# Performance work log

Measured on AMD Instinct MI355X. Metric: run time of the kernel, lower is better.

The kernel has to match this reference:

```python
import jax, jax.numpy as jnp
import numpy as np

N_NODES = 100000
N_EDGES = 1600000
HIDDEN = 128
NUM_CLASSES = 10
NUM_LAYERS = 4
NUM_GRAPHS = 200
BN_EPS = 1e-5


def setup_inputs() -> dict:
    key = jax.random.key(0)
    ks = jax.random.split(key, 16)
    s = 1.0 / np.sqrt(HIDDEN)
    inp = {
        "x": jax.random.normal(ks[0], (N_NODES, HIDDEN), jnp.float32),
        "edge_index": jax.random.randint(ks[1], (2, N_EDGES), 0, N_NODES, jnp.int64),
        "batch": jnp.sort(jax.random.randint(ks[2], (N_NODES,), 0, NUM_GRAPHS, jnp.int64)),
        # GatedGraphConv per-layer message weights [L, H, H]
        "ggnn_weight": jax.random.uniform(ks[3], (NUM_LAYERS, HIDDEN, HIDDEN), jnp.float32, -s, s),
        # shared GRUCell params (torch layout: [3H, H])
        "gru_w_ih": jax.random.uniform(ks[4], (3 * HIDDEN, HIDDEN), jnp.float32, -s, s),
        "gru_w_hh": jax.random.uniform(ks[5], (3 * HIDDEN, HIDDEN), jnp.float32, -s, s),
        "gru_b_ih": jax.random.uniform(ks[6], (3 * HIDDEN,), jnp.float32, -s, s),
        "gru_b_hh": jax.random.uniform(ks[7], (3 * HIDDEN,), jnp.float32, -s, s),
        "fc1_w": jax.random.uniform(ks[8], (HIDDEN, HIDDEN), jnp.float32, -s, s),
        "fc1_b": jax.random.uniform(ks[9], (HIDDEN,), jnp.float32, -s, s),
        "bn_gamma": jnp.ones((HIDDEN,), jnp.float32),
        "bn_beta": jnp.zeros((HIDDEN,), jnp.float32),
        "fc2_w": jax.random.uniform(ks[10], (NUM_CLASSES, HIDDEN), jnp.float32, -s, s),
        "fc2_b": jax.random.uniform(ks[11], (NUM_CLASSES,), jnp.float32, -s, s),
    }
    return inp


def _gru_cell(m, h, w_ih, w_hh, b_ih, b_hh):
    gi = m @ w_ih.T + b_ih  # [N, 3H]
    gh = h @ w_hh.T + b_hh
    i_r, i_z, i_n = jnp.split(gi, 3, axis=-1)
    h_r, h_z, h_n = jnp.split(gh, 3, axis=-1)
    r = jax.nn.sigmoid(i_r + h_r)
    z = jax.nn.sigmoid(i_z + h_z)
    n = jnp.tanh(i_n + r * h_n)
    return (1.0 - z) * n + z * h


def reference(x, edge_index, batch, ggnn_weight, gru_w_ih, gru_w_hh, gru_b_ih,
              gru_b_hh, fc1_w, fc1_b, bn_gamma, bn_beta, fc2_w, fc2_b):
    src, dst = edge_index[0], edge_index[1]
    h = x
    for l in range(NUM_LAYERS):
        m = h @ ggnn_weight[l]                       # [N, H] per-layer transform
        agg = jax.ops.segment_sum(m[src], dst, num_segments=N_NODES)  # scatter-add
        h = _gru_cell(agg, h, gru_w_ih, gru_w_hh, gru_b_ih, gru_b_hh)
    # fc1 -> batchnorm (training-mode batch stats) -> relu; dropout is identity (eval)
    y = h @ fc1_w.T + fc1_b
    mu = jnp.mean(y, axis=0)
    var = jnp.var(y, axis=0)
    y = (y - mu) * jax.lax.rsqrt(var + BN_EPS) * bn_gamma + bn_beta
    y = jax.nn.relu(y)
    # global mean pool per graph
    sums = jax.ops.segment_sum(y, batch, num_segments=NUM_GRAPHS)
    counts = jax.ops.segment_sum(jnp.ones((N_NODES,), y.dtype), batch, num_segments=NUM_GRAPHS)
    gfeat = sums / jnp.clip(counts, 1.0)[:, None]    # [G, H]
    out = gfeat @ fc2_w.T + fc2_b                    # [G, C]
    return jax.nn.log_softmax(out, axis=-1)
```

## Files before the change

### kernel.cpp

```cpp
#include <hip/hip_runtime.h>
#include <math.h>

#define HID 128
#define NLAYERS 4
#define NGRAPHS 200
#define NCLASSES 10
#define BN_EPS 1e-5f

typedef short bf16x8 __attribute__((ext_vector_type(8)));
typedef float f32x4 __attribute__((ext_vector_type(4)));

__device__ __forceinline__ ushort f2bf(float f) {
    unsigned u = __float_as_uint(f);
    u = (u + 0x7fffu + ((u >> 16) & 1u)) >> 16;
    return (ushort)u;
}
__device__ __forceinline__ float bf2f(unsigned us) { return __uint_as_float(us << 16); }


__global__ void k_init_x(const float* __restrict__ x, ushort* __restrict__ A, int N) {
    int idx = blockIdx.x * blockDim.x + threadIdx.x;
    if (idx < N * HID) {
        int n = idx >> 7, c = idx & 127;
        A[n * 256 + 128 + c] = f2bf(x[idx]);
    }
}

__global__ __launch_bounds__(128) void k_wgemm(const float* __restrict__ W,
                                               const float* __restrict__ w_ih,
                                               float* __restrict__ C) {
    int l = blockIdx.x >> 7, k = blockIdx.x & 127;
    __shared__ float wrow[128];
    wrow[threadIdx.x] = W[(l << 14) + k * 128 + threadIdx.x];
    __syncthreads();
    for (int j = threadIdx.x; j < 384; j += 128) {
        float acc = 0.f;
#pragma unroll 4
        for (int o = 0; o < 128; ++o) acc += wrow[o] * w_ih[j * 128 + o];
        C[((size_t)l * 128 + k) * 384 + j] = acc;
    }
}

__global__ void k_build_Bc(const float* __restrict__ C, const float* __restrict__ w_hh,
                           ushort* __restrict__ Bc2) {
    int idx = blockIdx.x * blockDim.x + threadIdx.x;
    if (idx >= NLAYERS * 512 * 256) return;
    int jf = idx & 7, lane = (idx >> 3) & 63, ks = (idx >> 9) & 7, ct = (idx >> 12) & 31;
    int l = idx >> 17;
    int o = ct * 16 + (lane & 15);
    int k = ks * 32 + (lane >> 4) * 8 + jf;
    float v;
    if (k < 128)      v = (o < 384) ? C[((size_t)l * 128 + k) * 384 + o] : 0.f;
    else if (o < 256) v = w_hh[o * 128 + (k - 128)];
    else if (o < 384) v = 0.f;
    else              v = w_hh[(o - 128) * 128 + (k - 128)];
    Bc2[idx] = f2bf(v);
}

__global__ void k_bias(const float* __restrict__ b_ih, const float* __restrict__ b_hh,
                       float* __restrict__ bias) {
    int j = threadIdx.x;
    if (j >= 512) return;
    float v;
    if (j < 256)      v = b_ih[j] + b_hh[j];
    else if (j < 384) v = b_ih[j];
    else              v = b_hh[j - 128];
    bias[j] = v;
}

__global__ void k_cvt_fc1(const float* __restrict__ w, ushort* __restrict__ B2) {
    int idx = blockIdx.x * blockDim.x + threadIdx.x;
    if (idx >= 16384) return;
    int j = idx & 7, lane = (idx >> 3) & 63, ks = (idx >> 9) & 3, ct = idx >> 11;
    int o = ct * 16 + (lane & 15);
    int k = ks * 32 + (lane >> 4) * 8 + j;
    B2[idx] = f2bf(w[o * 128 + k]);
}


__global__ void k_deg(const int* __restrict__ ei, int E, int* __restrict__ deg) {
    int e = blockIdx.x * blockDim.x + threadIdx.x;
    if (e < E) atomicAdd(&deg[ei[E + e]], 1);
}

__global__ void k_scan1(const int* __restrict__ deg, int N,
                        int* __restrict__ rowstart, int* __restrict__ bsum) {
    __shared__ int s[256];
    int t = threadIdx.x;
    int i = blockIdx.x * 256 + t;
    int v = (i < N) ? deg[i] : 0;
    s[t] = v;
    __syncthreads();
    for (int off = 1; off < 256; off <<= 1) {
        int a = (t >= off) ? s[t - off] : 0;
        __syncthreads();
        s[t] += a;
        __syncthreads();
    }
    if (i < N) rowstart[i] = s[t] - v;
    if (t == 255) bsum[blockIdx.x] = s[255];
}

__global__ void k_scan2(const int* __restrict__ bsum, int nb, int* __restrict__ boff) {
    __shared__ int s[512];
    int t = threadIdx.x;
    int v = (t < nb) ? bsum[t] : 0;
    s[t] = v;
    __syncthreads();
    for (int off = 1; off < 512; off <<= 1) {
        int a = (t >= off) ? s[t - off] : 0;
        __syncthreads();
        s[t] += a;
        __syncthreads();
    }
    if (t < nb) boff[t] = s[t] - v;
}

__global__ void k_scan3(int* __restrict__ rowstart, const int* __restrict__ boff,
                        int N, int E) {
    int i = blockIdx.x * 256 + threadIdx.x;
    if (i < N) rowstart[i] += boff[blockIdx.x];
    if (i == 0) rowstart[N] = E;
}

__global__ void k_fill(const int* __restrict__ ei, int E,
                       const int* __restrict__ rowstart, int* __restrict__ cursor,
                       int* __restrict__ col) {
    int e = blockIdx.x * blockDim.x + threadIdx.x;
    if (e < E) {
        int d = ei[E + e];
        int pos = atomicAdd(&cursor[d], 1);
        col[rowstart[d] + pos] = ei[e];
    }
}


__global__ void k_gstart(const int* __restrict__ batch, int* __restrict__ gstart, int N) {
    int n = blockIdx.x * blockDim.x + threadIdx.x;
    if (n > N) return;
    int curb = (n == N) ? NGRAPHS : batch[n];
    int prev = (n == 0) ? -1 : batch[n - 1];
    for (int g = prev + 1; g <= curb; ++g) gstart[g] = n;
}


__global__ __launch_bounds__(256) void k_gather_bf(const int* __restrict__ rowstart,
                                                   const int* __restrict__ col,
                                                   ushort* __restrict__ A, int N) {
    int node = blockIdx.x * 4 + (threadIdx.x >> 6);
    int lane = threadIdx.x & 63;
    if (node >= N) return;
    int s = rowstart[node], e = rowstart[node + 1];
    int sub = lane >> 4;
    int chunk = lane & 15;
    const ushort* hb = A + 128;
    float acc[8];
#pragma unroll
    for (int k = 0; k < 8; ++k) acc[k] = 0.f;
    int i = s + sub;
    for (; i + 12 < e; i += 16) {
        int c0 = col[i], c1 = col[i + 4], c2 = col[i + 8], c3 = col[i + 12];
        bf16x8 v0 = *(const bf16x8*)(hb + (size_t)c0 * 256 + chunk * 8);
        bf16x8 v1 = *(const bf16x8*)(hb + (size_t)c1 * 256 + chunk * 8);
        bf16x8 v2 = *(const bf16x8*)(hb + (size_t)c2 * 256 + chunk * 8);
        bf16x8 v3 = *(const bf16x8*)(hb + (size_t)c3 * 256 + chunk * 8);
#pragma unroll
        for (int k = 0; k < 8; ++k) {
            acc[k] += bf2f((ushort)v0[k]) + bf2f((ushort)v1[k]);
            acc[k] += bf2f((ushort)v2[k]) + bf2f((ushort)v3[k]);
        }
    }
    for (; i < e; i += 4) {
        int c0 = col[i];
        bf16x8 v0 = *(const bf16x8*)(hb + (size_t)c0 * 256 + chunk * 8);
#pragma unroll
        for (int k = 0; k < 8; ++k) acc[k] += bf2f((ushort)v0[k]);
    }
#pragma unroll
    for (int k = 0; k < 8; ++k) {
        acc[k] += __shfl_xor(acc[k], 16);
        acc[k] += __shfl_xor(acc[k], 32);
    }
    if (sub == 0) {
        union { ushort u[8]; bf16x8 v; } o;
#pragma unroll
        for (int k = 0; k < 8; ++k) o.u[k] = f2bf(acc[k]);
        *(bf16x8*)(A + (size_t)node * 256 + chunk * 8) = o.v;
    }
}


#define LDA 264
__global__ __launch_bounds__(256, 2) void k_gru_mfma(
    const ushort* __restrict__ A, const ushort* __restrict__ Bc2,
    const float* __restrict__ bias, ushort* __restrict__ Ah) {
    __shared__ ushort As[64 * LDA];
    int t = threadIdx.x;
    int rowb = blockIdx.x << 6;
    for (int c = t; c < 2048; c += 256) {
        int r = c >> 5, off = (c & 31) * 8;
        *(bf16x8*)(As + r * LDA + off) =
            *(const bf16x8*)(A + (size_t)(rowb + r) * 256 + off);
    }
    __syncthreads();
    int w = t >> 6, lane = t & 63;
    int quad = lane >> 4, tn = lane & 15;
    f32x4 acc[4][4][2];
#pragma unroll
    for (int rt = 0; rt < 4; ++rt)
#pragma unroll
        for (int g = 0; g < 4; ++g)
#pragma unroll
            for (int c2 = 0; c2 < 2; ++c2) acc[rt][g][c2] = (f32x4){0.f, 0.f, 0.f, 0.f};
    for (int ks = 0; ks < 8; ++ks) {
        int k0 = ks * 32 + quad * 8;
        bf16x8 bfr[4][2];
#pragma unroll
        for (int g = 0; g < 4; ++g)
#pragma unroll
            for (int c2 = 0; c2 < 2; ++c2) {
                int ct = g * 8 + w * 2 + c2;
                bfr[g][c2] = *(const bf16x8*)(Bc2 + (size_t)((ct * 8 + ks) * 64 + lane) * 8);
            }
        bf16x8 af[4];
#pragma unroll
        for (int rt = 0; rt < 4; ++rt)
            af[rt] = *(const bf16x8*)(As + (rt * 16 + tn) * LDA + k0);
#pragma unroll
        for (int rt = 0; rt < 4; ++rt)
#pragma unroll
            for (int g = 0; g < 4; ++g)
#pragma unroll
                for (int c2 = 0; c2 < 2; ++c2)
                    acc[rt][g][c2] = __builtin_amdgcn_mfma_f32_16x16x32_bf16(
                        af[rt], bfr[g][c2], acc[rt][g][c2], 0, 0, 0);
    }
#pragma unroll
    for (int c2 = 0; c2 < 2; ++c2) {
        int cc = w * 32 + c2 * 16 + tn;
        float br = bias[cc], bz = bias[128 + cc], bin = bias[256 + cc], bhn = bias[384 + cc];
#pragma unroll
        for (int rt = 0; rt < 4; ++rt)
#pragma unroll
            for (int r = 0; r < 4; ++r) {
                int rl = rt * 16 + quad * 4 + r;
                int row = rowb + rl;
                float ur = acc[rt][0][c2][r] + br;
                float uz = acc[rt][1][c2][r] + bz;
                float xin = acc[rt][2][c2][r] + bin;
                float xhn = acc[rt][3][c2][r] + bhn;
                float rr = 1.f / (1.f + __expf(-ur));
                float zz = 1.f / (1.f + __expf(-uz));
                float xt = xin + rr * xhn;
                float ex = __expf(2.f * fminf(fmaxf(xt, -15.f), 15.f));
                float nn = (ex - 1.f) / (ex + 1.f);
                float ho = bf2f(As[rl * LDA + 128 + cc]);
                float hv = (1.f - zz) * nn + zz * ho;
                Ah[(size_t)row * 256 + cc] = f2bf(hv);
            }
    }
}


#define LDA2 136
__global__ __launch_bounds__(256, 2) void k_mm_mfma(
    const ushort* __restrict__ Ain, int astride, const ushort* __restrict__ B2,
    ushort* __restrict__ mo) {
    __shared__ ushort As[64 * LDA2];
    int t = threadIdx.x;
    int rowb = blockIdx.x << 6;
    for (int c = t; c < 1024; c += 256) {
        int r = c >> 4, off = (c & 15) * 8;
        *(bf16x8*)(As + r * LDA2 + off) =
            *(const bf16x8*)(Ain + (size_t)(rowb + r) * astride + off);
    }
    __syncthreads();
    int w = t >> 6, lane = t & 63;
    int quad = lane >> 4, tn = lane & 15;
    f32x4 acc[4][2];
#pragma unroll
    for (int rt = 0; rt < 4; ++rt)
#pragma unroll
        for (int c2 = 0; c2 < 2; ++c2) acc[rt][c2] = (f32x4){0.f, 0.f, 0.f, 0.f};
    for (int ks = 0; ks < 4; ++ks) {
        int k0 = ks * 32 + quad * 8;
        bf16x8 bfr[2];
#pragma unroll
        for (int c2 = 0; c2 < 2; ++c2) {
            int ct = w * 2 + c2;
            bfr[c2] = *(const bf16x8*)(B2 + (size_t)((ct * 4 + ks) * 64 + lane) * 8);
        }
        bf16x8 af[4];
#pragma unroll
        for (int rt = 0; rt < 4; ++rt)
            af[rt] = *(const bf16x8*)(As + (rt * 16 + tn) * LDA2 + k0);
#pragma unroll
        for (int rt = 0; rt < 4; ++rt)
#pragma unroll
            for (int c2 = 0; c2 < 2; ++c2)
                acc[rt][c2] = __builtin_amdgcn_mfma_f32_16x16x32_bf16(
                    af[rt], bfr[c2], acc[rt][c2], 0, 0, 0);
    }
#pragma unroll
    for (int c2 = 0; c2 < 2; ++c2) {
        int col = w * 32 + c2 * 16 + tn;
#pragma unroll
        for (int rt = 0; rt < 4; ++rt)
#pragma unroll
            for (int r = 0; r < 4; ++r) {
                int row = rowb + rt * 16 + quad * 4 + r;
                mo[row * 128 + col] = f2bf(acc[rt][c2][r]);
            }
    }
}


__global__ __launch_bounds__(256) void k_bnstats(const ushort* __restrict__ y,
                                                 float* __restrict__ stats, int N) {
    int half = threadIdx.x >> 7, f = threadIdx.x & 127;
    float s = 0.f, s2 = 0.f;
    for (int n = blockIdx.x * 2 + half; n < N; n += gridDim.x * 2) {
        float v = bf2f(y[n * HID + f]);
        s += v;
        s2 += v * v;
    }
    __shared__ float ls[2][HID], ls2[2][HID];
    ls[half][f] = s;
    ls2[half][f] = s2;
    __syncthreads();
    if (half == 0) {
        atomicAdd(&stats[f], ls[0][f] + ls[1][f]);
        atomicAdd(&stats[HID + f], ls2[0][f] + ls2[1][f]);
    }
}

__global__ void k_bnfinal(float* __restrict__ stats, const float* __restrict__ gamma,
                          const float* __restrict__ beta, float n) {
    int j = threadIdx.x;
    if (j < HID) {
        float mu = stats[j] / n;
        float var = stats[HID + j] / n - mu * mu;
        float sc = gamma[j] * rsqrtf(var + BN_EPS);
        stats[256 + j] = sc;
        stats[384 + j] = beta[j] - mu * sc;
    }
}

__global__ __launch_bounds__(256) void k_pool(const ushort* __restrict__ y,
                                              const float* __restrict__ stats,
                                              const int* __restrict__ gstart,
                                              float* __restrict__ gsum) {
    int g = blockIdx.x >> 2, q = blockIdx.x & 3;
    int f = threadIdx.x & 127, half = threadIdx.x >> 7;
    int gs = gstart[g], ge = gstart[g + 1];
    int len = ge - gs;
    int r0 = gs + ((len * q) >> 2), r1 = gs + ((len * (q + 1)) >> 2);
    float sc = stats[256 + f], sh = stats[384 + f];
    float acc = 0.f;
    for (int n = r0 + half; n < r1; n += 2)
        acc += fmaxf(bf2f(y[n * HID + f]) * sc + sh, 0.f);
    __shared__ float ls[2][HID];
    ls[half][f] = acc;
    __syncthreads();
    if (half == 0) atomicAdd(&gsum[g * HID + f], ls[0][f] + ls[1][f]);
}

__global__ void k_head(const float* __restrict__ gsum, const int* __restrict__ gstart,
                       const float* __restrict__ w2, const float* __restrict__ b2,
                       float* __restrict__ out) {
    int g = blockIdx.x * blockDim.x + threadIdx.x;
    if (g >= NGRAPHS) return;
    float cnt = (float)(gstart[g + 1] - gstart[g]);
    float inv = 1.0f / fmaxf(cnt, 1.0f);
    float logits[NCLASSES];
    float mx = -1e30f;
    for (int c = 0; c < NCLASSES; ++c) {
        float acc = b2[c];
        for (int f = 0; f < HID; ++f) acc += gsum[g * HID + f] * inv * w2[c * HID + f];
        logits[c] = acc;
        mx = fmaxf(mx, acc);
    }
    float se = 0.f;
    for (int c = 0; c < NCLASSES; ++c) se += expf(logits[c] - mx);
    float lse = mx + logf(se);
    for (int c = 0; c < NCLASSES; ++c) out[g * NCLASSES + c] = logits[c] - lse;
}


extern "C" void kernel_launch(void* const* d_in, const int* in_sizes, int n_in,
                              void* d_out, int out_size, void* d_ws, size_t ws_size,
                              hipStream_t stream) {
    const float* x     = (const float*)d_in[0];
    const int*   ei    = (const int*)d_in[1];
    const int*   batch = (const int*)d_in[2];
    const float* ggnnw = (const float*)d_in[3];
    const float* w_ih  = (const float*)d_in[4];
    const float* w_hh  = (const float*)d_in[5];
    const float* b_ih  = (const float*)d_in[6];
    const float* b_hh  = (const float*)d_in[7];
    const float* fc1_w = (const float*)d_in[8];
    const float* gamma = (const float*)d_in[10];
    const float* beta  = (const float*)d_in[11];
    const float* fc2_w = (const float*)d_in[12];
    const float* fc2_b = (const float*)d_in[13];
    float* out = (float*)d_out;

    const int N = in_sizes[0] / HID;
    const int E = in_sizes[1] / 2;
    const int nblk64 = (N + 63) / 64;
    const int P = nblk64 * 64;

    char* w = (char*)d_ws;
    auto alloc = [&](size_t bytes) -> char* {
        char* p = w;
        w += (bytes + 255) & ~(size_t)255;
        return p;
    };
    ushort* A   = (ushort*)alloc(sizeof(ushort) * (size_t)P * 256);
    ushort* y   = (ushort*)alloc(sizeof(ushort) * (size_t)P * HID);
    ushort* Bc2 = (ushort*)alloc(sizeof(ushort) * NLAYERS * 512 * 256);
    float*  C   = (float*)alloc(sizeof(float) * NLAYERS * 128 * 384);
    ushort* f1b = (ushort*)alloc(sizeof(ushort) * HID * HID);
    float*  bias = (float*)alloc(sizeof(float) * 512);
    int* rowstart = (int*)alloc(sizeof(int) * (N + 4));
    int* colb     = (int*)alloc(sizeof(int) * E);
    int* bsum     = (int*)alloc(sizeof(int) * 512);
    int* boff     = (int*)alloc(sizeof(int) * 512);
    int* gstart   = (int*)alloc(sizeof(int) * (NGRAPHS + 4));
    size_t zelems = (size_t)N + N + 512 + NGRAPHS * HID;
    char* zbase = alloc(zelems * 4);
    int*   deg    = (int*)zbase;
    int*   cursor = deg + N;
    float* stats  = (float*)(cursor + N);
    float* gsum   = stats + 512;

    hipMemsetAsync(zbase, 0, zelems * 4, stream);

    k_init_x<<<(N * HID + 255) / 256, 256, 0, stream>>>(x, A, N);
    k_wgemm<<<NLAYERS * 128, 128, 0, stream>>>(ggnnw, w_ih, C);
    k_build_Bc<<<(NLAYERS * 512 * 256 + 255) / 256, 256, 0, stream>>>(C, w_hh, Bc2);
    k_bias<<<1, 512, 0, stream>>>(b_ih, b_hh, bias);
    k_cvt_fc1<<<(16384 + 255) / 256, 256, 0, stream>>>(fc1_w, f1b);

    int nb1 = (N + 255) / 256;
    k_deg<<<(E + 255) / 256, 256, 0, stream>>>(ei, E, deg);
    k_scan1<<<nb1, 256, 0, stream>>>(deg, N, rowstart, bsum);
    k_scan2<<<1, 512, 0, stream>>>(bsum, nb1, boff);
    k_scan3<<<nb1, 256, 0, stream>>>(rowstart, boff, N, E);
    k_fill<<<(E + 255) / 256, 256, 0, stream>>>(ei, E, rowstart, cursor, colb);
    k_gstart<<<(N + 256) / 256, 256, 0, stream>>>(batch, gstart, N);

    for (int l = 0; l < NLAYERS; ++l) {
        k_gather_bf<<<(N + 3) / 4, 256, 0, stream>>>(rowstart, colb, A, N);
        k_gru_mfma<<<nblk64, 256, 0, stream>>>(A, Bc2 + (size_t)l * 512 * 256,
                                               bias, A + 128);
    }

    k_mm_mfma<<<nblk64, 256, 0, stream>>>(A + 128, 256, f1b, y);
    k_bnstats<<<512, 256, 0, stream>>>(y, stats, N);
    k_bnfinal<<<1, 128, 0, stream>>>(stats, gamma, beta, (float)N);
    k_pool<<<NGRAPHS * 4, 256, 0, stream>>>(y, stats, gstart, gsum);
    k_head<<<1, 256, 0, stream>>>(gsum, gstart, fc2_w, fc2_b, out);
}
```

Before: 851.0 us.

## Build CSR via two-level bucketed counting sort instead of global atomics

```diff
diff --git a/kernel.cpp b/kernel.cpp
--- a/kernel.cpp
+++ b/kernel.cpp
@@ -78,17 +78,26 @@
 }
 
 
-__global__ void k_deg(const int* __restrict__ ei, int E, int* __restrict__ deg) {
-    int e = blockIdx.x * blockDim.x + threadIdx.x;
-    if (e < E) atomicAdd(&deg[ei[E + e]], 1);
-}
-
-__global__ void k_scan1(const int* __restrict__ deg, int N,
-                        int* __restrict__ rowstart, int* __restrict__ bsum) {
+#define CHUNK 4096
+
+__global__ __launch_bounds__(256) void k_bhist(const int* __restrict__ ei, int E,
+                                               int nb, int* __restrict__ bhist) {
+    __shared__ int lh[256];
+    int t = threadIdx.x;
+    lh[t] = 0;
+    __syncthreads();
+    int base = blockIdx.x * CHUNK;
+    int end = min(base + CHUNK, E);
+    for (int i = base + t; i < end; i += 256) atomicAdd(&lh[ei[E + i] >> 9], 1);
+    __syncthreads();
+    if (t < nb && lh[t]) atomicAdd(&bhist[t], lh[t]);
+}
+
+__global__ void k_bscan(const int* __restrict__ bhist, int nb, int* __restrict__ bstart,
+                        int* __restrict__ bcur, int E) {
     __shared__ int s[256];
     int t = threadIdx.x;
-    int i = blockIdx.x * 256 + t;
-    int v = (i < N) ? deg[i] : 0;
+    int v = (t < nb) ? bhist[t] : 0;
     s[t] = v;
     __syncthreads();
     for (int off = 1; off < 256; off <<= 1) {
@@ -97,41 +106,90 @@
         s[t] += a;
         __syncthreads();
     }
-    if (i < N) rowstart[i] = s[t] - v;
-    if (t == 255) bsum[blockIdx.x] = s[255];
-}
-
-__global__ void k_scan2(const int* __restrict__ bsum, int nb, int* __restrict__ boff) {
-    __shared__ int s[512];
+    if (t < nb) { int ex = s[t] - v; bstart[t] = ex; bcur[t] = ex; }
+    if (t == 0) bstart[nb] = E;
+}
+
+__global__ __launch_bounds__(256) void k_binfill(const int* __restrict__ ei, int E,
+                                                 int nb, int* __restrict__ bcur,
+                                                 int2* __restrict__ binned) {
+    __shared__ int eh[256], eoff[256], ecur[256], gbase[256];
+    __shared__ int2 sbuf[CHUNK];
     int t = threadIdx.x;
-    int v = (t < nb) ? bsum[t] : 0;
-    s[t] = v;
+    eh[t] = 0; ecur[t] = 0;
+    __syncthreads();
+    int base = blockIdx.x * CHUNK;
+    int cnt = min(CHUNK, E - base);
+    int2 ed[16];
+    int nmine = 0;
+    for (int i = t; i < cnt; i += 256) {
+        int s = ei[base + i], d = ei[E + base + i];
+        ed[nmine++] = make_int2(s, d);
+        atomicAdd(&eh[d >> 9], 1);
+    }
+    __syncthreads();
+    int v = eh[t];
+    eoff[t] = v;
+    __syncthreads();
+    for (int off = 1; off < 256; off <<= 1) {
+        int a = (t >= off) ? eoff[t - off] : 0;
+        __syncthreads();
+        eoff[t] += a;
+        __syncthreads();
+    }
+    int excl = eoff[t] - v;
+    __syncthreads();
+    eoff[t] = excl;
+    __syncthreads();
+    for (int j = 0; j < nmine; ++j) {
+        int b = ed[j].y >> 9;
+        int slot = eoff[b] + atomicAdd(&ecur[b], 1);
+        sbuf[slot] = ed[j];
+    }
+    __syncthreads();
+    if (t < nb && eh[t]) gbase[t] = atomicAdd(&bcur[t], eh[t]);
+    __syncthreads();
+    for (int i = t; i < cnt; i += 256) {
+        int2 e = sbuf[i];
+        int b = e.y >> 9;
+        binned[gbase[b] + (i - eoff[b])] = e;
+    }
+}
+
+__global__ __launch_bounds__(256) void k_csr512(const int2* __restrict__ binned,
+                                                const int* __restrict__ bstart,
+                                                int* __restrict__ rowstart,
+                                                int* __restrict__ col, int N, int E) {
+    __shared__ int h[512], cur[512], sc[512];
+    int t = threadIdx.x, b = blockIdx.x;
+    int es = bstart[b], ee = bstart[b + 1];
+    for (int i = t; i < 512; i += 256) h[i] = 0;
+    __syncthreads();
+    for (int i = es + t; i < ee; i += 256) atomicAdd(&h[binned[i].y & 511], 1);
+    __syncthreads();
+    for (int i = t; i < 512; i += 256) sc[i] = h[i];
     __syncthreads();
     for (int off = 1; off < 512; off <<= 1) {
-        int a = (t >= off) ? s[t - off] : 0;
+        int i0 = t, i1 = t + 256;
+        int a0 = (i0 >= off) ? sc[i0 - off] : 0;
+        int a1 = (i1 >= off) ? sc[i1 - off] : 0;
         __syncthreads();
-        s[t] += a;
+        sc[i0] += a0; sc[i1] += a1;
         __syncthreads();
     }
-    if (t < nb) boff[t] = s[t] - v;
-}
-
-__global__ void k_scan3(int* __restrict__ rowstart, const int* __restrict__ boff,
-                        int N, int E) {
-    int i = blockIdx.x * 256 + threadIdx.x;
-    if (i < N) rowstart[i] += boff[blockIdx.x];
-    if (i == 0) rowstart[N] = E;
-}
-
-__global__ void k_fill(const int* __restrict__ ei, int E,
-                       const int* __restrict__ rowstart, int* __restrict__ cursor,
-                       int* __restrict__ col) {
-    int e = blockIdx.x * blockDim.x + threadIdx.x;
-    if (e < E) {
-        int d = ei[E + e];
-        int pos = atomicAdd(&cursor[d], 1);
-        col[rowstart[d] + pos] = ei[e];
-    }
+    for (int i = t; i < 512; i += 256) {
+        int excl = sc[i] - h[i];
+        cur[i] = excl;
+        int node = (b << 9) + i;
+        if (node < N) rowstart[node] = es + excl;
+    }
+    __syncthreads();
+    for (int i = es + t; i < ee; i += 256) {
+        int2 e = binned[i];
+        int p = atomicAdd(&cur[e.y & 511], 1);
+        col[es + p] = e.x;
+    }
+    if (b == 0 && t == 0) rowstart[N] = E;
 }
 
 
@@ -409,6 +467,7 @@
     const int E = in_sizes[1] / 2;
     const int nblk64 = (N + 63) / 64;
     const int P = nblk64 * 64;
+    const int nbuck = (N + 511) >> 9;
 
     char* w = (char*)d_ws;
     auto alloc = [&](size_t bytes) -> char* {
@@ -418,20 +477,20 @@
     };
     ushort* A   = (ushort*)alloc(sizeof(ushort) * (size_t)P * 256);
     ushort* y   = (ushort*)alloc(sizeof(ushort) * (size_t)P * HID);
+    int2*   binned = (int2*)y;
     ushort* Bc2 = (ushort*)alloc(sizeof(ushort) * NLAYERS * 512 * 256);
     float*  C   = (float*)alloc(sizeof(float) * NLAYERS * 128 * 384);
     ushort* f1b = (ushort*)alloc(sizeof(ushort) * HID * HID);
     float*  bias = (float*)alloc(sizeof(float) * 512);
     int* rowstart = (int*)alloc(sizeof(int) * (N + 4));
     int* colb     = (int*)alloc(sizeof(int) * E);
-    int* bsum     = (int*)alloc(sizeof(int) * 512);
-    int* boff     = (int*)alloc(sizeof(int) * 512);
+    int* bstart   = (int*)alloc(sizeof(int) * (nbuck + 4));
+    int* bcur     = (int*)alloc(sizeof(int) * (nbuck + 4));
     int* gstart   = (int*)alloc(sizeof(int) * (NGRAPHS + 4));
-    size_t zelems = (size_t)N + N + 512 + NGRAPHS * HID;
+    size_t zelems = (size_t)nbuck + 512 + NGRAPHS * HID;
     char* zbase = alloc(zelems * 4);
-    int*   deg    = (int*)zbase;
-    int*   cursor = deg + N;
-    float* stats  = (float*)(cursor + N);
+    int*   bhist  = (int*)zbase;
+    float* stats  = (float*)(bhist + nbuck);
     float* gsum   = stats + 512;
 
     hipMemsetAsync(zbase, 0, zelems * 4, stream);
@@ -442,12 +501,11 @@
     k_bias<<<1, 512, 0, stream>>>(b_ih, b_hh, bias);
     k_cvt_fc1<<<(16384 + 255) / 256, 256, 0, stream>>>(fc1_w, f1b);
 
-    int nb1 = (N + 255) / 256;
-    k_deg<<<(E + 255) / 256, 256, 0, stream>>>(ei, E, deg);
-    k_scan1<<<nb1, 256, 0, stream>>>(deg, N, rowstart, bsum);
-    k_scan2<<<1, 512, 0, stream>>>(bsum, nb1, boff);
-    k_scan3<<<nb1, 256, 0, stream>>>(rowstart, boff, N, E);
-    k_fill<<<(E + 255) / 256, 256, 0, stream>>>(ei, E, rowstart, cursor, colb);
+    int nchunk = (E + CHUNK - 1) / CHUNK;
+    k_bhist<<<nchunk, 256, 0, stream>>>(ei, E, nbuck, bhist);
+    k_bscan<<<1, 256, 0, stream>>>(bhist, nbuck, bstart, bcur, E);
+    k_binfill<<<nchunk, 256, 0, stream>>>(ei, E, nbuck, bcur, binned);
+    k_csr512<<<nbuck, 256, 0, stream>>>(binned, bstart, rowstart, colb, N, E);
     k_gstart<<<(N + 256) / 256, 256, 0, stream>>>(batch, gstart, N);
 
     for (int l = 0; l < NLAYERS; ++l) {
```

Result: faster. 771.3 us (-9.4%).
